# Kernel optimization log

Measured on AMD Instinct MI355X. Metric: run time of the kernel, lower is better.

Reference implementation:

```python
import jax, jax.numpy as jnp
import numpy as np

B, T, D, H = 2, 2048, 1024, 16
HD = D // H

def setup_inputs() -> dict:
    key = jax.random.key(0)
    ks = jax.random.split(key, 5)
    fan = D
    bound_w = float(np.sqrt(6.0 / fan))  # kaiming_uniform-ish scale
    return {
        "x": jax.random.normal(ks[0], (B, T, D), dtype=jnp.float32),
        "W_qkv": jax.random.uniform(ks[1], (3 * D, D), minval=-bound_w, maxval=bound_w, dtype=jnp.float32),
        "b_qkv": jax.random.uniform(ks[2], (3 * D,), minval=-bound_w, maxval=bound_w, dtype=jnp.float32),
        "W_proj": jax.random.uniform(ks[3], (D, D), minval=-bound_w, maxval=bound_w, dtype=jnp.float32),
        "b_proj": jax.random.uniform(ks[4], (D,), minval=-bound_w, maxval=bound_w, dtype=jnp.float32),
    }

def reference(x, W_qkv, b_qkv, W_proj, b_proj):
    Bx, Tx, C = x.shape
    h, hd = H, C // H
    qkv = x @ W_qkv.T + b_qkv                      # (B,T,3C)
    q, k, v = jnp.split(qkv, 3, axis=-1)
    # (B,T,C) -> (B,h,T,hd)
    q = q.reshape(Bx, Tx, h, hd).transpose(0, 2, 1, 3)
    k = k.reshape(Bx, Tx, h, hd).transpose(0, 2, 1, 3)
    v = v.reshape(Bx, Tx, h, hd).transpose(0, 2, 1, 3)
    scale = hd ** -0.5
    scores = jnp.einsum('bhqd,bhkd->bhqk', q, k) * scale
    causal = jnp.tril(jnp.ones((Tx, Tx), dtype=bool))
    scores = jnp.where(causal, scores, -jnp.inf)
    weights = jax.nn.softmax(scores, axis=-1)      # stable softmax, same math
    out = jnp.einsum('bhqk,bhkd->bhqd', weights, v)
    out = out.transpose(0, 2, 1, 3).reshape(Bx, Tx, C)
    return out @ W_proj.T + b_proj
```

## Files before the change

### kernel.cpp

```cpp
#include <hip/hip_runtime.h>

typedef unsigned short u16;
typedef __attribute__((ext_vector_type(8))) short bf16x8;
typedef __attribute__((ext_vector_type(4))) float f32x4;

#define Bb 2
#define Tt 2048
#define Dd 1024
#define Hh 16
#define HD 64
#define NTOK (Bb*Tt)
#define QKVN (3*Dd)

__device__ __forceinline__ u16 f2b(float f) {
    unsigned u = __float_as_uint(f);
    unsigned r = (u + 0x7fffu + ((u >> 16) & 1u)) >> 16;
    return (u16)r;
}

__device__ __forceinline__ void g2l16(const u16* g, u16* l) {
    __builtin_amdgcn_global_load_lds(
        (const __attribute__((address_space(1))) unsigned int*)g,
        (__attribute__((address_space(3))) unsigned int*)l,
        16, 0, 0);
}

__device__ __forceinline__ unsigned pk2(float lo, float hi) {
    return __builtin_amdgcn_perm(__float_as_uint(hi), __float_as_uint(lo), 0x07060302u);
}

#define N4X  (NTOK * Dd / 4)
#define N4WQ (3 * Dd * Dd / 4)
#define N4WP (Dd * Dd / 4)
__global__ void cvt_all(const float* __restrict__ x, const float* __restrict__ wq,
                        const float* __restrict__ wp, u16* __restrict__ xb,
                        u16* __restrict__ wqb, u16* __restrict__ wpb) {
    int i = blockIdx.x * blockDim.x + threadIdx.x;
    const float* src; u16* dst; int j;
    if (i < N4X)                { src = x;  dst = xb;  j = i; }
    else if (i < N4X + N4WQ)    { src = wq; dst = wqb; j = i - N4X; }
    else                        { src = wp; dst = wpb; j = i - N4X - N4WQ; }
    float4 f = ((const float4*)src)[j];
    ushort4 o;
    o.x = f2b(f.x); o.y = f2b(f.y); o.z = f2b(f.z); o.w = f2b(f.w);
    ((ushort4*)dst)[j] = o;
}

#define TRS 136

__global__ __launch_bounds__(256, 3)
void gemm_qkv(const u16* __restrict__ A, const u16* __restrict__ Bt,
              const float* __restrict__ bias,
              u16* __restrict__ C16, u16* __restrict__ Vt) {
    const int N = QKVN, K = Dd;
    __shared__ alignas(16) u16 smem[128 * TRS];
    u16* As = smem;
    u16* Bs = smem + 8192;
    const int tid = threadIdx.x;
    const int wave = tid >> 6, lane = tid & 63;
    const int quad = lane >> 4, l16 = lane & 15;
    const int wm = (wave & 1) * 64, wn = (wave >> 1) * 64;
    const int m0 = blockIdx.x * 128, n0 = blockIdx.y * 128;
    const int lrow = lane >> 2, lcol = (lane & 3) << 3;

    f32x4 acc[4][4];
#pragma unroll
    for (int i = 0; i < 4; ++i)
#pragma unroll
        for (int j = 0; j < 4; ++j)
            acc[i][j] = (f32x4){0.f, 0.f, 0.f, 0.f};

    for (int k0 = 0; k0 < K; k0 += 64) {
#pragma unroll
        for (int h = 0; h < 2; ++h)
#pragma unroll
            for (int c = 0; c < 2; ++c) {
                const int rb = (c * 4 + wave) * 16;
                g2l16(A  + (size_t)(m0 + rb + lrow) * K + k0 + h * 32 + lcol,
                      &As[h * 4096 + rb * 32 + (lane << 3)]);
                g2l16(Bt + (size_t)(n0 + rb + lrow) * K + k0 + h * 32 + lcol,
                      &Bs[h * 4096 + rb * 32 + (lane << 3)]);
            }
        __syncthreads();
        bf16x8 a[4][2], b[4][2];
#pragma unroll
        for (int h = 0; h < 2; ++h) {
#pragma unroll
            for (int i = 0; i < 4; ++i)
                a[i][h] = *(const bf16x8*)(&As[h * 4096 + (wm + i * 16 + l16) * 32 + quad * 8]);
#pragma unroll
            for (int i = 0; i < 4; ++i)
                b[i][h] = *(const bf16x8*)(&Bs[h * 4096 + (wn + i * 16 + l16) * 32 + quad * 8]);
        }
#pragma unroll
        for (int h = 0; h < 2; ++h)
#pragma unroll
            for (int i = 0; i < 4; ++i)
#pragma unroll
                for (int j = 0; j < 4; ++j)
                    acc[i][j] = __builtin_amdgcn_mfma_f32_16x16x32_bf16(a[i][h], b[j][h], acc[i][j], 0, 0, 0);
        __syncthreads();
    }

    float b4[4];
#pragma unroll
    for (int j = 0; j < 4; ++j) b4[j] = bias[n0 + wn + j * 16 + l16];
    const bool isV = (n0 >= 2 * Dd);

    if (!isV) {
#pragma unroll
        for (int i = 0; i < 4; ++i)
#pragma unroll
            for (int j = 0; j < 4; ++j)
#pragma unroll
                for (int r = 0; r < 4; ++r) {
                    int m = m0 + wm + i * 16 + quad * 4 + r;
                    int n = n0 + wn + j * 16 + l16;
                    C16[(size_t)m * N + n] = f2b(acc[i][j][r] + b4[j]);
                }
    } else {
#pragma unroll
        for (int i = 0; i < 4; ++i)
#pragma unroll
            for (int j = 0; j < 4; ++j)
#pragma unroll
                for (int r = 0; r < 4; ++r) {
                    int ml = wm + i * 16 + quad * 4 + r;
                    int nl = wn + j * 16 + l16;
                    smem[nl * TRS + ml] = f2b(acc[i][j][r] + b4[j]);
                }
        __syncthreads();
        const int bidx = m0 >> 11, t0 = m0 & 2047;
        const int nl = tid >> 1, toff = (tid & 1) * 64;
        u16* dst = Vt + (size_t)bidx * (Hh * HD * Tt)
                      + (size_t)(n0 - 2 * Dd + nl) * Tt + t0 + toff;
        const u16* srcl = &smem[nl * TRS + toff];
#pragma unroll
        for (int k = 0; k < 8; ++k)
            *(uint4*)(dst + k * 8) = *(const uint4*)(srcl + k * 8);
    }
}

__global__ __launch_bounds__(256, 2)
void gemm_proj(const u16* __restrict__ A, const u16* __restrict__ Bt,
               const float* __restrict__ bias, float* __restrict__ Co) {
    const int N = Dd, K = Dd;
    __shared__ alignas(16) u16 As[2 * 128 * 32];
    __shared__ alignas(16) u16 Bs[2 * 64 * 32];
    const int tid = threadIdx.x;
    const int wave = tid >> 6, lane = tid & 63;
    const int quad = lane >> 4, l16 = lane & 15;
    const int wm = (wave & 1) * 64, wn = (wave >> 1) * 32;
    const int m0 = blockIdx.x * 128, n0 = blockIdx.y * 64;
    const int lrow = lane >> 2, lcol = (lane & 3) << 3;

    f32x4 acc[4][2];
#pragma unroll
    for (int i = 0; i < 4; ++i)
#pragma unroll
        for (int j = 0; j < 2; ++j)
            acc[i][j] = (f32x4){0.f, 0.f, 0.f, 0.f};

    for (int k0 = 0; k0 < K; k0 += 64) {
#pragma unroll
        for (int h = 0; h < 2; ++h) {
#pragma unroll
            for (int c = 0; c < 2; ++c) {
                const int rb = (c * 4 + wave) * 16;
                g2l16(A + (size_t)(m0 + rb + lrow) * K + k0 + h * 32 + lcol,
                      &As[h * 4096 + rb * 32 + (lane << 3)]);
            }
            g2l16(Bt + (size_t)(n0 + wave * 16 + lrow) * K + k0 + h * 32 + lcol,
                  &Bs[h * 2048 + (wave * 16) * 32 + (lane << 3)]);
        }
        __syncthreads();
        bf16x8 a[4][2], b[2][2];
#pragma unroll
        for (int h = 0; h < 2; ++h) {
#pragma unroll
            for (int i = 0; i < 4; ++i)
                a[i][h] = *(const bf16x8*)(&As[h * 4096 + (wm + i * 16 + l16) * 32 + quad * 8]);
#pragma unroll
            for (int j = 0; j < 2; ++j)
                b[j][h] = *(const bf16x8*)(&Bs[h * 2048 + (wn + j * 16 + l16) * 32 + quad * 8]);
        }
#pragma unroll
        for (int h = 0; h < 2; ++h)
#pragma unroll
            for (int i = 0; i < 4; ++i)
#pragma unroll
                for (int j = 0; j < 2; ++j)
                    acc[i][j] = __builtin_amdgcn_mfma_f32_16x16x32_bf16(a[i][h], b[j][h], acc[i][j], 0, 0, 0);
        __syncthreads();
    }

    float b2[2];
#pragma unroll
    for (int j = 0; j < 2; ++j) b2[j] = bias[n0 + wn + j * 16 + l16];

#pragma unroll
    for (int i = 0; i < 4; ++i)
#pragma unroll
        for (int j = 0; j < 2; ++j)
#pragma unroll
            for (int r = 0; r < 4; ++r) {
                int m = m0 + wm + i * 16 + quad * 4 + r;
                int n = n0 + wn + j * 16 + l16;
                Co[(size_t)m * N + n] = acc[i][j][r] + b2[j];
            }
}

#define LKP 80
#define PSP 84
#define FMX 24.0f

__global__ __launch_bounds__(256, 3)
void attn_fwd(const u16* __restrict__ qkv, const u16* __restrict__ Vt,
              u16* __restrict__ Ao) {
    const int bid = blockIdx.x;
    const int xcd = bid & 7, li = bid >> 3;
    const int bh = (xcd << 2) | (li & 3);
    const int qt = 31 - (li >> 2);
    const int hh = bh & (Hh - 1), bidx = bh >> 4;
    const u16* Qp = qkv + (size_t)bidx * Tt * QKVN + hh * HD;
    const u16* Kp = Qp + Dd;
    const u16* Vp = Vt + (size_t)bh * HD * Tt;
    const int tid = threadIdx.x;
    const int wave = tid >> 6, lane = tid & 63;
    const int quad = lane >> 4, l16 = lane & 15;

    __shared__ alignas(16) u16 Ks[2][64 * LKP];
    __shared__ alignas(16) u16 Vs[2][64 * LKP];
    __shared__ alignas(16) u16 Ps[4][16 * PSP];
    u16* Pw = &Ps[wave][0];

    const int srow = tid >> 3, scol = (tid & 7) << 3;
    const int st0 = srow * LKP + scol, st1 = (srow + 32) * LKP + scol;
    const float sc = 0.125f * 1.44269504f;

    float mb[16];
#pragma unroll
    for (int nt = 0; nt < 4; ++nt)
#pragma unroll
        for (int r = 0; r < 4; ++r)
            mb[nt * 4 + r] = (nt * 16 + quad * 4 + r <= wave * 16 + l16) ? -FMX : -250.0f;

    const int qrow_g = qt * 64 + wave * 16 + l16;
    bf16x8 aq[2];
#pragma unroll
    for (int kk = 0; kk < 2; ++kk)
        aq[kk] = *(const bf16x8*)(Qp + (size_t)qrow_g * QKVN + kk * 32 + quad * 8);

    f32x4 o[4];
#pragma unroll
    for (int nt = 0; nt < 4; ++nt) o[nt] = (f32x4){0.f, 0.f, 0.f, 0.f};
    float lsum = 0.f;

    {
        uint4 k0r = *(const uint4*)(Kp + (size_t)srow * QKVN + scol);
        uint4 k1r = *(const uint4*)(Kp + (size_t)(srow + 32) * QKVN + scol);
        uint4 v0r = *(const uint4*)(Vp + (size_t)srow * Tt + scol);
        uint4 v1r = *(const uint4*)(Vp + (size_t)(srow + 32) * Tt + scol);
        *(uint4*)(&Ks[0][st0]) = k0r;
        *(uint4*)(&Ks[0][st1]) = k1r;
        *(uint4*)(&Vs[0][st0]) = v0r;
        *(uint4*)(&Vs[0][st1]) = v1r;
    }
    __syncthreads();

    const u16* kp0 = Kp + (size_t)(64 + srow) * QKVN + scol;
    const u16* kp1 = kp0 + (size_t)32 * QKVN;
    const u16* vp0 = Vp + (size_t)srow * Tt + 64 + scol;
    const u16* vp1 = vp0 + (size_t)32 * Tt;

    u16* Kcur = &Ks[0][0]; u16* Knxt = &Ks[1][0];
    u16* Vcur = &Vs[0][0]; u16* Vnxt = &Vs[1][0];

    for (int kt = 0; kt < qt; ++kt) {
        uint4 k0r = *(const uint4*)kp0;
        uint4 k1r = *(const uint4*)kp1;
        uint4 v0r = *(const uint4*)vp0;
        uint4 v1r = *(const uint4*)vp1;
        kp0 += (size_t)64 * QKVN; kp1 += (size_t)64 * QKVN;
        vp0 += 64; vp1 += 64;

        f32x4 s[4];
#pragma unroll
        for (int nt = 0; nt < 4; ++nt) {
            f32x4 z = (f32x4){0.f, 0.f, 0.f, 0.f};
#pragma unroll
            for (int kk = 0; kk < 2; ++kk) {
                bf16x8 ak = *(const bf16x8*)(&Kcur[(nt * 16 + l16) * LKP + kk * 32 + quad * 8]);
                z = __builtin_amdgcn_mfma_f32_16x16x32_bf16(ak, aq[kk], z, 0, 0, 0);
            }
            s[nt] = z;
        }

#pragma unroll
        for (int nt = 0; nt < 4; ++nt)
#pragma unroll
            for (int r = 0; r < 4; ++r) {
                float p = exp2f(__builtin_fmaf(s[nt][r], sc, -FMX));
                s[nt][r] = p;
                lsum += p;
            }

#pragma unroll
        for (int nt = 0; nt < 4; ++nt) {
            uint2 d;
            d.x = pk2(s[nt][0], s[nt][1]);
            d.y = pk2(s[nt][2], s[nt][3]);
            *(uint2*)(&Pw[l16 * PSP + nt * 16 + quad * 4]) = d;
        }

#pragma unroll
        for (int kk = 0; kk < 2; ++kk) {
            bf16x8 bp = *(const bf16x8*)(&Pw[l16 * PSP + kk * 32 + quad * 8]);
#pragma unroll
            for (int nt = 0; nt < 4; ++nt) {
                bf16x8 av = *(const bf16x8*)(&Vcur[(nt * 16 + l16) * LKP + kk * 32 + quad * 8]);
                o[nt] = __builtin_amdgcn_mfma_f32_16x16x32_bf16(av, bp, o[nt], 0, 0, 0);
            }
        }

        *(uint4*)(&Knxt[st0]) = k0r;
        *(uint4*)(&Knxt[st1]) = k1r;
        *(uint4*)(&Vnxt[st0]) = v0r;
        *(uint4*)(&Vnxt[st1]) = v1r;
        u16* t;
        t = Kcur; Kcur = Knxt; Knxt = t;
        t = Vcur; Vcur = Vnxt; Vnxt = t;
        __syncthreads();
    }

    {
        f32x4 s[4];
#pragma unroll
        for (int nt = 0; nt < 4; ++nt) {
            f32x4 z = (f32x4){0.f, 0.f, 0.f, 0.f};
#pragma unroll
            for (int kk = 0; kk < 2; ++kk) {
                bf16x8 ak = *(const bf16x8*)(&Kcur[(nt * 16 + l16) * LKP + kk * 32 + quad * 8]);
                z = __builtin_amdgcn_mfma_f32_16x16x32_bf16(ak, aq[kk], z, 0, 0, 0);
            }
            s[nt] = z;
        }
#pragma unroll
        for (int nt = 0; nt < 4; ++nt)
#pragma unroll
            for (int r = 0; r < 4; ++r) {
                float p = exp2f(__builtin_fmaf(s[nt][r], sc, mb[nt * 4 + r]));
                s[nt][r] = p;
                lsum += p;
            }
#pragma unroll
        for (int nt = 0; nt < 4; ++nt) {
            uint2 d;
            d.x = pk2(s[nt][0], s[nt][1]);
            d.y = pk2(s[nt][2], s[nt][3]);
            *(uint2*)(&Pw[l16 * PSP + nt * 16 + quad * 4]) = d;
        }
#pragma unroll
        for (int kk = 0; kk < 2; ++kk) {
            bf16x8 bp = *(const bf16x8*)(&Pw[l16 * PSP + kk * 32 + quad * 8]);
#pragma unroll
            for (int nt = 0; nt < 4; ++nt) {
                bf16x8 av = *(const bf16x8*)(&Vcur[(nt * 16 + l16) * LKP + kk * 32 + quad * 8]);
                o[nt] = __builtin_amdgcn_mfma_f32_16x16x32_bf16(av, bp, o[nt], 0, 0, 0);
            }
        }
    }

    lsum += __shfl_xor(lsum, 16, 64);
    lsum += __shfl_xor(lsum, 32, 64);
    const float rinv = 1.0f / lsum;
    u16* orow = Ao + ((size_t)bidx * Tt + qrow_g) * Dd + hh * HD;
#pragma unroll
    for (int nt = 0; nt < 4; ++nt) {
        ushort4 p4;
        p4.x = f2b(o[nt][0] * rinv); p4.y = f2b(o[nt][1] * rinv);
        p4.z = f2b(o[nt][2] * rinv); p4.w = f2b(o[nt][3] * rinv);
        *(ushort4*)(orow + nt * 16 + quad * 4) = p4;
    }
}

extern "C" void kernel_launch(void* const* d_in, const int* in_sizes, int n_in,
                              void* d_out, int out_size, void* d_ws, size_t ws_size,
                              hipStream_t stream) {
    const float* x      = (const float*)d_in[0];
    const float* W_qkv  = (const float*)d_in[1];
    const float* b_qkv  = (const float*)d_in[2];
    const float* W_proj = (const float*)d_in[3];
    const float* b_proj = (const float*)d_in[4];
    float* out = (float*)d_out;

    char* ws = (char*)d_ws;
    u16* Wprojb = (u16*)(ws);
    u16* Wqkvb  = (u16*)(ws + (2u << 20));
    u16* xb     = (u16*)(ws + (8u << 20));
    u16* qkvb   = (u16*)(ws + (16u << 20));
    u16* Vtb    = (u16*)(ws + (40u << 20));
    u16* attnb  = (u16*)(ws + (2u << 20));

    cvt_all<<<(N4X + N4WQ + N4WP) / 256, 256, 0, stream>>>(x, W_qkv, W_proj, xb, Wqkvb, Wprojb);

    {
        dim3 grid(NTOK / 128, QKVN / 128);
        gemm_qkv<<<grid, 256, 0, stream>>>(xb, Wqkvb, b_qkv, qkvb, Vtb);
    }
    {
        attn_fwd<<<dim3(1024), 256, 0, stream>>>(qkvb, Vtb, attnb);
    }
    {
        dim3 grid(NTOK / 128, Dd / 64);
        gemm_proj<<<grid, 256, 0, stream>>>(attnb, Wprojb, b_proj, out);
    }
}
```

Before: 178.3 us.

## Keep P in registers via 16x16x16 MFMA, drop LDS staging, rebalance causal tiles

The softmax probabilities are packed to bf16 and fed straight into 16x16x16 MFMA instructions from registers, so the LDS round trip through a per-wave P buffer goes away. The block-to-(head, query-tile) mapping is changed to interleave heavy and light causal tiles across the blocks on each XCD. Launch bounds are raised to 4 blocks per CU, which is possible now that less shared memory is used. The tradeoff is twice as many, smaller MFMA ops with 8-byte V reads from LDS, and a tighter register budget from the higher occupancy target.

```diff
diff --git a/kernel.cpp b/kernel.cpp
--- a/kernel.cpp
+++ b/kernel.cpp
@@ -2,6 +2,7 @@
 
 typedef unsigned short u16;
 typedef __attribute__((ext_vector_type(8))) short bf16x8;
+typedef __attribute__((ext_vector_type(4))) short bf16x4;
 typedef __attribute__((ext_vector_type(4))) float f32x4;
 
 #define Bb 2
@@ -211,16 +212,18 @@
 }
 
 #define LKP 80
-#define PSP 84
 #define FMX 24.0f
 
-__global__ __launch_bounds__(256, 3)
+__global__ __launch_bounds__(256, 4)
 void attn_fwd(const u16* __restrict__ qkv, const u16* __restrict__ Vt,
               u16* __restrict__ Ao) {
     const int bid = blockIdx.x;
     const int xcd = bid & 7, li = bid >> 3;
-    const int bh = (xcd << 2) | (li & 3);
-    const int qt = 31 - (li >> 2);
+    const int bsub = li >> 5;
+    const int vz = li & 31;
+    const int zz = (vz & 1) ? (vz >> 1) : (31 - (vz >> 1));
+    const int qt = (bsub & 1) ? (31 - zz) : zz;
+    const int bh = (xcd << 2) | bsub;
     const int hh = bh & (Hh - 1), bidx = bh >> 4;
     const u16* Qp = qkv + (size_t)bidx * Tt * QKVN + hh * HD;
     const u16* Kp = Qp + Dd;
@@ -231,8 +234,6 @@
 
     __shared__ alignas(16) u16 Ks[2][64 * LKP];
     __shared__ alignas(16) u16 Vs[2][64 * LKP];
-    __shared__ alignas(16) u16 Ps[4][16 * PSP];
-    u16* Pw = &Ps[wave][0];
 
     const int srow = tid >> 3, scol = (tid & 7) << 3;
     const int st0 = srow * LKP + scol, st1 = (srow + 32) * LKP + scol;
@@ -305,23 +306,22 @@
                 lsum += p;
             }
 
+        bf16x4 ps[4];
 #pragma unroll
         for (int nt = 0; nt < 4; ++nt) {
-            uint2 d;
-            d.x = pk2(s[nt][0], s[nt][1]);
-            d.y = pk2(s[nt][2], s[nt][3]);
-            *(uint2*)(&Pw[l16 * PSP + nt * 16 + quad * 4]) = d;
-        }
-
-#pragma unroll
-        for (int kk = 0; kk < 2; ++kk) {
-            bf16x8 bp = *(const bf16x8*)(&Pw[l16 * PSP + kk * 32 + quad * 8]);
-#pragma unroll
-            for (int nt = 0; nt < 4; ++nt) {
-                bf16x8 av = *(const bf16x8*)(&Vcur[(nt * 16 + l16) * LKP + kk * 32 + quad * 8]);
-                o[nt] = __builtin_amdgcn_mfma_f32_16x16x32_bf16(av, bp, o[nt], 0, 0, 0);
-            }
-        }
+            uint2 w;
+            w.x = pk2(s[nt][0], s[nt][1]);
+            w.y = pk2(s[nt][2], s[nt][3]);
+            ps[nt] = *(bf16x4*)&w;
+        }
+
+#pragma unroll
+        for (int nt = 0; nt < 4; ++nt)
+#pragma unroll
+            for (int ntO = 0; ntO < 4; ++ntO) {
+                bf16x4 av = *(const bf16x4*)(&Vcur[(ntO * 16 + l16) * LKP + nt * 16 + quad * 4]);
+                o[ntO] = __builtin_amdgcn_mfma_f32_16x16x16bf16_1k(av, ps[nt], o[ntO], 0, 0, 0);
+            }
 
         *(uint4*)(&Knxt[st0]) = k0r;
         *(uint4*)(&Knxt[st1]) = k1r;
@@ -353,22 +353,21 @@
                 s[nt][r] = p;
                 lsum += p;
             }
+        bf16x4 ps[4];
 #pragma unroll
         for (int nt = 0; nt < 4; ++nt) {
-            uint2 d;
-            d.x = pk2(s[nt][0], s[nt][1]);
-            d.y = pk2(s[nt][2], s[nt][3]);
-            *(uint2*)(&Pw[l16 * PSP + nt * 16 + quad * 4]) = d;
-        }
-#pragma unroll
-        for (int kk = 0; kk < 2; ++kk) {
-            bf16x8 bp = *(const bf16x8*)(&Pw[l16 * PSP + kk * 32 + quad * 8]);
-#pragma unroll
-            for (int nt = 0; nt < 4; ++nt) {
-                bf16x8 av = *(const bf16x8*)(&Vcur[(nt * 16 + l16) * LKP + kk * 32 + quad * 8]);
-                o[nt] = __builtin_amdgcn_mfma_f32_16x16x32_bf16(av, bp, o[nt], 0, 0, 0);
-            }
-        }
+            uint2 w;
+            w.x = pk2(s[nt][0], s[nt][1]);
+            w.y = pk2(s[nt][2], s[nt][3]);
+            ps[nt] = *(bf16x4*)&w;
+        }
+#pragma unroll
+        for (int nt = 0; nt < 4; ++nt)
+#pragma unroll
+            for (int ntO = 0; ntO < 4; ++ntO) {
+                bf16x4 av = *(const bf16x4*)(&Vcur[(ntO * 16 + l16) * LKP + nt * 16 + quad * 4]);
+                o[ntO] = __builtin_amdgcn_mfma_f32_16x16x16bf16_1k(av, ps[nt], o[ntO], 0, 0, 0);
+            }
     }
 
     lsum += __shfl_xor(lsum, 16, 64);
```

New measurement: 180.1 us. No clear change (+1.0%).
